# Performance work log

Hardware: AMD Instinct MI355X
Metric: run time of the kernel (lower is better)

## Reference

```python
import jax, jax.numpy as jnp
import numpy as np

HIDDEN = 128

def setup_inputs() -> dict:
    key = jax.random.key(0)
    ks = jax.random.split(key, 12)
    N, T, H = 4096, 64, HIDDEN
    s_in = 1.0 / np.sqrt(2.0)
    s_h = 1.0 / np.sqrt(H)
    return {
        "x_seq": jax.random.normal(ks[0], (N, T), dtype=jnp.float32),
        "m_seq": jax.random.uniform(ks[1], (N, T), dtype=jnp.float32),
        # linear layers stored as [in, out] (math identical to torch x @ W.T + b)
        "W_in": jax.random.normal(ks[2], (2, H), dtype=jnp.float32) * s_in,
        "b_in": jax.random.normal(ks[3], (H,), dtype=jnp.float32) * 0.01,
        "W_proj": jax.random.normal(ks[4], (H, H), dtype=jnp.float32) * s_h,
        "b_proj": jax.random.normal(ks[5], (H,), dtype=jnp.float32) * 0.01,
        "W_gcn": jax.random.normal(ks[6], (H, H), dtype=jnp.float32) * s_h,
        "b_gcn": jax.random.normal(ks[7], (H,), dtype=jnp.float32) * 0.01,
        "W_out": jax.random.normal(ks[8], (H, 1), dtype=jnp.float32) * s_h,
        "b_out": jax.random.normal(ks[9], (1,), dtype=jnp.float32) * 0.01,
    }


def reference(x_seq, m_seq, W_in, b_in, W_proj, b_proj, W_gcn, b_gcn, W_out, b_out):
    N, T = x_seq.shape
    H = W_in.shape[1]
    scale = 1.0 / jnp.sqrt(jnp.asarray(H, dtype=x_seq.dtype))
    # [T, N, 2] time-major inputs for scan
    xs = jnp.stack([x_seq, m_seq], axis=-1).transpose(1, 0, 2)
    h0 = jnp.zeros((N, H), dtype=x_seq.dtype)

    def step(h, inp_t):
        h_in = jax.nn.relu(inp_t @ W_in + b_in)            # [N, H]
        h_proj = h @ W_proj + b_proj                        # [N, H]
        A_dyn = jax.nn.softmax(h_proj @ h_proj.T * scale, axis=1)  # [N, N]
        msg = A_dyn @ h_in                                  # [N, H]
        h_new = jax.nn.relu(msg @ W_gcn + b_gcn + h_in)     # [N, H]
        pred = (h_new @ W_out + b_out)[:, 0]                # [N]
        return h_new, pred

    _, preds = jax.lax.scan(step, h0, xs)  # preds: [T, N]
    return preds.T  # [N, T]
```

## Files before the change

### kernel.cpp

```cpp
#include <hip/hip_runtime.h>
#include <math.h>

#define NN 4096
#define TT 64
#define HH 128
#define NNP 4160
#define SLICE (128 * NNP)
#define SPLITS 8
#define KPB (NN / SPLITS)
#define KT 64
#define NTILES (KPB / KT)
#define QB 64
#define SCALE 0.08838834764831845f
#define CSHIFT 16.0f

typedef __attribute__((ext_vector_type(8))) short short8;
typedef __attribute__((ext_vector_type(4))) float f32x4;
typedef unsigned long long u64;
#define MFMA(a, b, c)   __builtin_amdgcn_mfma_f32_16x16x32_bf16((a), (b), (c), 0, 0, 0)

__device__ __forceinline__ short f2b(float f) {
    union { float f; unsigned u; } v; v.f = f;
    unsigned r = v.u + 0x7fffu + ((v.u >> 16) & 1u);
    return (short)(r >> 16);
}
__device__ __forceinline__ float b2f(short s) {
    union { unsigned u; float f; } v; v.u = ((unsigned)(unsigned short)s) << 16;
    return v.f;
}
__device__ __forceinline__ void lds_fence() {
    __asm__ __volatile__("s_waitcnt lgkmcnt(0)" ::: "memory");
}


__global__ __launch_bounds__(256) void prep_kernel(
    const float* __restrict__ x_seq, const float* __restrict__ m_seq,
    const float* __restrict__ W_in,  const float* __restrict__ b_in,
    const float* __restrict__ W_proj,const float* __restrict__ b_proj,
    const float* __restrict__ W_gcn,
    short* __restrict__ hp, short* __restrict__ hinT_all,
    short* __restrict__ WgT, short* __restrict__ WpT)
{
    __shared__ __align__(16) short hb[128 * 66];
    const int b = blockIdx.x, tid = threadIdx.x;
    if (b < 256) {
        const int n0 = b * 16;
        for (int i = tid; i < 16 * HH; i += 256) {
            const int q = i >> 7, j = i & 127, n = n0 + q;
            hp[n * HH + j] = f2b(b_proj[j]);
        }
    } else if (b < 272) {
        const int wb = b - 256;
        #pragma unroll
        for (int k = 0; k < 4; ++k) {
            const int idx = wb * 1024 + k * 256 + tid;
            const int n = idx >> 7, kk = idx & 127;
            WgT[idx] = f2b(W_gcn[kk * HH + n]);
            WpT[idx] = f2b(W_proj[kk * HH + n]);
        }
    } else {
        const int u = b - 272;
        const int t = u >> 6, n0 = (u & 63) * 64;
        for (int i = tid; i < 64 * HH; i += 256) {
            const int q = i >> 7, j = i & 127, n = n0 + q;
            float hv = x_seq[n * TT + t] * W_in[j] + m_seq[n * TT + t] * W_in[HH + j] + b_in[j];
            hv = hv > 0.f ? hv : 0.f;
            hb[j * 66 + q] = f2b(hv);
        }
        __syncthreads();
        short* dst = hinT_all + (size_t)t * SLICE;
        for (int c = tid; c < 128 * 16; c += 256) {
            const int j = c >> 4, off = (c & 15) * 4;
            const int nb = n0 + off;
            const int tcol = (nb & ~31) | (((nb >> 2) & 3) << 3) | (((nb >> 4) & 1) << 2);
            const unsigned lo = *(const unsigned*)&hb[j * 66 + off];
            const unsigned hi = *(const unsigned*)&hb[j * 66 + off + 2];
            const u64 v = (u64)lo | ((u64)hi << 32);
            *(u64*)&dst[(size_t)j * NNP + tcol] = v;
        }
    }
}

__global__ __launch_bounds__(256, 2) void attn_kernel(
    const short* __restrict__ hp, const short* __restrict__ hinT,
    short* __restrict__ OpartB, float* __restrict__ lpart)
{
    __shared__ __align__(16) char pool[71680];
    short* KtS = (short*)pool;
    short* VtS = (short*)(pool + 34816);

    const int tid  = threadIdx.x;
    const int wave = tid >> 6, lane = tid & 63;
    const int ln = lane & 15, g = lane >> 4;
    const int split = blockIdx.x >> 6, qg = blockIdx.x & 63;
    const int q0 = qg * QB + wave * 16;
    const int kbase = split * KPB;

    const int krow = tid >> 4, kcol = (tid & 15) * 8;
    const int vrow = tid >> 3, vcol = (tid & 7) * 8;

    short8 qf[4];
    #pragma unroll
    for (int kc = 0; kc < 4; ++kc)
        qf[kc] = *(const short8*)&hp[(q0 + ln) * HH + kc * 32 + g * 8];

    f32x4 oacc[8] = {};
    f32x4 lacc = {};
    short8 vone;
    #pragma unroll
    for (int e = 0; e < 8; ++e) vone[e] = (short)0x3F80;

    short8 ksA[4], vsA[4];
    auto load_tile = [&](int kt_) {
        const int kb = kbase + kt_ * KT;
        #pragma unroll
        for (int k = 0; k < 4; ++k)
            ksA[k] = *(const short8*)&hp[(kb + krow + 16 * k) * HH + kcol];
        #pragma unroll
        for (int k = 0; k < 4; ++k)
            vsA[k] = *(const short8*)&hinT[(size_t)(vrow + 32 * k) * NNP + kb + vcol];
    };
    auto store_tile = [&](int b) {
        #pragma unroll
        for (int k = 0; k < 4; ++k)
            *(short8*)&KtS[b * 8704 + (krow + 16 * k) * 136 + kcol] = ksA[k];
        #pragma unroll
        for (int k = 0; k < 4; ++k)
            *(short8*)&VtS[b * 9216 + (vrow + 32 * k) * 72 + vcol] = vsA[k];
    };

    load_tile(0);
    store_tile(0);

    for (int kt = 0; kt < NTILES; ++kt) {
        const int b = kt & 1;
        __syncthreads();

        short8 kf[4][4];
        #pragma unroll
        for (int kt2 = 0; kt2 < 4; ++kt2)
            #pragma unroll
            for (int kc = 0; kc < 4; ++kc)
                kf[kt2][kc] = *(const short8*)&KtS[b * 8704 + (kt2 * 16 + ln) * 136 + kc * 32 + g * 8];

        if (kt + 1 < NTILES) load_tile(kt + 1);

        f32x4 st[4] = {};
        __builtin_amdgcn_s_setprio(1);
        #pragma unroll
        for (int kt2 = 0; kt2 < 4; ++kt2)
            #pragma unroll
            for (int kc = 0; kc < 4; ++kc)
                st[kt2] = MFMA(kf[kt2][kc], qf[kc], st[kt2]);
        __builtin_amdgcn_s_setprio(0);

        short8 pa[2];
        #pragma unroll
        for (int p = 0; p < 2; ++p) {
            short8 paq;
            #pragma unroll
            for (int e = 0; e < 8; ++e) {
                const float s = (e < 4) ? st[2 * p][e] : st[2 * p + 1][e - 4];
                paq[e] = f2b(__expf(s * SCALE - CSHIFT));
            }
            pa[p] = paq;
        }

        if (kt + 1 < NTILES) store_tile(b ^ 1);

        #pragma unroll
        for (int p = 0; p < 2; ++p) {
            short8 vf[8];
            #pragma unroll
            for (int dt = 0; dt < 8; ++dt)
                vf[dt] = *(const short8*)&VtS[b * 9216 + (dt * 16 + ln) * 72 + p * 32 + g * 8];
            __builtin_amdgcn_s_setprio(1);
            #pragma unroll
            for (int dt = 0; dt < 8; ++dt)
                oacc[dt] = MFMA(pa[p], vf[dt], oacc[dt]);
            lacc = MFMA(pa[p], vone, lacc);
            __builtin_amdgcn_s_setprio(0);
        }
    }

    __syncthreads();

    if (ln == 0) {
        #pragma unroll
        for (int r = 0; r < 4; ++r)
            lpart[split * NN + q0 + g * 4 + r] = lacc[r];
    }

    short* bounce = (short*)pool + wave * 2048;
    #pragma unroll
    for (int dt = 0; dt < 8; ++dt)
        #pragma unroll
        for (int r = 0; r < 4; ++r)
            bounce[(g * 4 + r) * 128 + dt * 16 + ln] = f2b(oacc[dt][r]);
    lds_fence();
    #pragma unroll
    for (int sub = 0; sub < 4; ++sub) {
        const int qrow = sub * 4 + (lane >> 4), chunk = lane & 15;
        const short8 rd = *(const short8*)&bounce[qrow * 128 + chunk * 8];
        *(short8*)&OpartB[((size_t)split * NN + q0 + qrow) * HH + chunk * 8] = rd;
    }
}

__global__ __launch_bounds__(512) void fuse_kernel(
    const short* __restrict__ OpartB, const float* __restrict__ lpart,
    short* __restrict__ hp,
    const short* __restrict__ WgT, const short* __restrict__ WpT,
    const float* __restrict__ b_gcn, const float* __restrict__ b_proj,
    const float* __restrict__ W_out, const float* __restrict__ b_out,
    const float* __restrict__ x_seq, const float* __restrict__ m_seq,
    const float* __restrict__ W_in,  const float* __restrict__ b_in,
    float* __restrict__ out, int t)
{
    __shared__ __align__(16) short msgb[16 * 136];
    __shared__ __align__(16) short hnb[16 * 136];
    __shared__ float larr[16];
    __shared__ float ppd[8 * 16];

    const int tid = threadIdx.x;
    const int wave = tid >> 6, lane = tid & 63;
    const int ln = lane & 15, g = lane >> 4;
    const int fb = blockIdx.x;
    const int qg64 = (fb & 7) + 8 * (fb >> 5);
    const int qb = qg64 * 64 + ((fb >> 3) & 3) * 16;

    if (tid < 16) {
        float l = 0.f;
        #pragma unroll
        for (int sp = 0; sp < SPLITS; ++sp) l += lpart[sp * NN + qb + tid];
        larr[tid] = 1.0f / l;
    }
    __syncthreads();

    if (tid < 256) {
        const int q = tid >> 4, c8 = (tid & 15) * 8;
        float s[8] = {0.f, 0.f, 0.f, 0.f, 0.f, 0.f, 0.f, 0.f};
        #pragma unroll
        for (int sp = 0; sp < SPLITS; ++sp) {
            const short8 v = *(const short8*)&OpartB[((size_t)sp * NN + qb + q) * HH + c8];
            #pragma unroll
            for (int k = 0; k < 8; ++k) s[k] += b2f(v[k]);
        }
        const float inv = larr[q];
        short* mp = &msgb[q * 136 + c8];
        #pragma unroll
        for (int k = 0; k < 8; ++k) mp[k] = f2b(s[k] * inv);
    }
    __syncthreads();

    {
        short8 af[4];
        #pragma unroll
        for (int kc = 0; kc < 4; ++kc)
            af[kc] = *(const short8*)&msgb[ln * 136 + kc * 32 + g * 8];
        f32x4 c = {};
        #pragma unroll
        for (int kc = 0; kc < 4; ++kc)
            c = MFMA(af[kc], *(const short8*)&WgT[(wave * 16 + ln) * HH + kc * 32 + g * 8], c);
        const int j = wave * 16 + ln;
        const float bg = b_gcn[j], wo = W_out[j];
        const float wj0 = W_in[j], wj1 = W_in[HH + j], bj = b_in[j];
        float pr[4];
        #pragma unroll
        for (int r = 0; r < 4; ++r) {
            const int q = g * 4 + r;
            float hv = x_seq[(qb + q) * TT + t] * wj0 + m_seq[(qb + q) * TT + t] * wj1 + bj;
            hv = hv > 0.f ? hv : 0.f;
            float v = c[r] + bg + b2f(f2b(hv));
            v = v > 0.f ? v : 0.f;
            hnb[q * 136 + j] = f2b(v);
            pr[r] = v * wo;
        }
        #pragma unroll
        for (int r = 0; r < 4; ++r) {
            float p = pr[r];
            p += __shfl_xor(p, 1); p += __shfl_xor(p, 2);
            p += __shfl_xor(p, 4); p += __shfl_xor(p, 8);
            if (ln == 0) ppd[wave * 16 + g * 4 + r] = p;
        }
    }
    __syncthreads();

    if (tid < 16) {
        float s = b_out[0];
        #pragma unroll
        for (int w = 0; w < 8; ++w) s += ppd[w * 16 + tid];
        out[(qb + tid) * TT + t] = s;
    }

    if (t < TT - 1) {
        short8 hf[4];
        #pragma unroll
        for (int kc = 0; kc < 4; ++kc)
            hf[kc] = *(const short8*)&hnb[ln * 136 + kc * 32 + g * 8];
        f32x4 c = {};
        #pragma unroll
        for (int kc = 0; kc < 4; ++kc)
            c = MFMA(hf[kc], *(const short8*)&WpT[(wave * 16 + ln) * HH + kc * 32 + g * 8], c);
        const float bp = b_proj[wave * 16 + ln];
        #pragma unroll
        for (int r = 0; r < 4; ++r)
            hp[(qb + g * 4 + r) * HH + wave * 16 + ln] = f2b(c[r] + bp);
    }
}

extern "C" void kernel_launch(void* const* d_in, const int* in_sizes, int n_in,
                              void* d_out, int out_size, void* d_ws, size_t ws_size,
                              hipStream_t stream) {
    const float* x_seq  = (const float*)d_in[0];
    const float* m_seq  = (const float*)d_in[1];
    const float* W_in   = (const float*)d_in[2];
    const float* b_in   = (const float*)d_in[3];
    const float* W_proj = (const float*)d_in[4];
    const float* b_proj = (const float*)d_in[5];
    const float* W_gcn  = (const float*)d_in[6];
    const float* b_gcn  = (const float*)d_in[7];
    const float* W_out  = (const float*)d_in[8];
    const float* b_out  = (const float*)d_in[9];
    float* out = (float*)d_out;

    char* base = (char*)d_ws;
    const size_t MB = 1 << 20;
    short* hp       = (short*)(base + 0 * MB);
    short* WgT      = (short*)(base + 3 * MB);
    short* WpT      = (short*)(base + 3 * MB + 32768);
    float* lpart    = (float*)(base + 3 * MB + 65536);
    short* OpartB   = (short*)(base + 4 * MB);
    short* hinT_all = (short*)(base + 32 * MB);

    prep_kernel<<<272 + 64 * 64, 256, 0, stream>>>(x_seq, m_seq, W_in, b_in,
                                                   W_proj, b_proj, W_gcn,
                                                   hp, hinT_all, WgT, WpT);

    for (int t = 0; t < TT; ++t) {
        const short* hinT_t = hinT_all + (size_t)t * SLICE;
        attn_kernel<<<(NN / QB) * SPLITS, 256, 0, stream>>>(hp, hinT_t, OpartB, lpart);
        fuse_kernel<<<NN / 16, 512, 0, stream>>>(OpartB, lpart, hp,
                                                 WgT, WpT, b_gcn, b_proj, W_out, b_out,
                                                 x_seq, m_seq, W_in, b_in, out, t);
    }
}
```

Baseline: 1.545 ms.

## Process two query tiles per wave and double key splits in attention

Each wave now handles 32 query rows (two 16-row tiles) instead of 16, so every K/V fragment read from LDS feeds twice as many MFMAs. The QK and PV phases are interleaved per 32-key half, which keeps the score registers small. The key dimension is split 16 ways instead of 8 to keep the grid size the same. In exchange, register pressure rises from doubled accumulators, and the fuse kernel must reduce twice as many partial outputs.

```diff
diff --git a/kernel.cpp b/kernel.cpp
--- a/kernel.cpp
+++ b/kernel.cpp
@@ -6,11 +6,11 @@
 #define HH 128
 #define NNP 4160
 #define SLICE (128 * NNP)
-#define SPLITS 8
+#define SPLITS 16
 #define KPB (NN / SPLITS)
 #define KT 64
 #define NTILES (KPB / KT)
-#define QB 64
+#define QB 128
 #define SCALE 0.08838834764831845f
 #define CSHIFT 16.0f
 
@@ -92,20 +92,22 @@
     const int tid  = threadIdx.x;
     const int wave = tid >> 6, lane = tid & 63;
     const int ln = lane & 15, g = lane >> 4;
-    const int split = blockIdx.x >> 6, qg = blockIdx.x & 63;
-    const int q0 = qg * QB + wave * 16;
+    const int split = blockIdx.x >> 5, qg = blockIdx.x & 31;
+    const int q0 = qg * QB + wave * 32;
     const int kbase = split * KPB;
 
     const int krow = tid >> 4, kcol = (tid & 15) * 8;
     const int vrow = tid >> 3, vcol = (tid & 7) * 8;
 
-    short8 qf[4];
+    short8 qf[2][4];
     #pragma unroll
-    for (int kc = 0; kc < 4; ++kc)
-        qf[kc] = *(const short8*)&hp[(q0 + ln) * HH + kc * 32 + g * 8];
-
-    f32x4 oacc[8] = {};
-    f32x4 lacc = {};
+    for (int qt = 0; qt < 2; ++qt)
+        #pragma unroll
+        for (int kc = 0; kc < 4; ++kc)
+            qf[qt][kc] = *(const short8*)&hp[(q0 + qt * 16 + ln) * HH + kc * 32 + g * 8];
+
+    f32x4 oacc[2][8] = {};
+    f32x4 lacc[2] = {};
     short8 vone;
     #pragma unroll
     for (int e = 0; e < 8; ++e) vone[e] = (short)0x3F80;
@@ -136,73 +138,84 @@
         const int b = kt & 1;
         __syncthreads();
 
-        short8 kf[4][4];
-        #pragma unroll
-        for (int kt2 = 0; kt2 < 4; ++kt2)
-            #pragma unroll
-            for (int kc = 0; kc < 4; ++kc)
-                kf[kt2][kc] = *(const short8*)&KtS[b * 8704 + (kt2 * 16 + ln) * 136 + kc * 32 + g * 8];
-
         if (kt + 1 < NTILES) load_tile(kt + 1);
 
-        f32x4 st[4] = {};
-        __builtin_amdgcn_s_setprio(1);
-        #pragma unroll
-        for (int kt2 = 0; kt2 < 4; ++kt2)
-            #pragma unroll
-            for (int kc = 0; kc < 4; ++kc)
-                st[kt2] = MFMA(kf[kt2][kc], qf[kc], st[kt2]);
-        __builtin_amdgcn_s_setprio(0);
-
-        short8 pa[2];
         #pragma unroll
         for (int p = 0; p < 2; ++p) {
-            short8 paq;
-            #pragma unroll
-            for (int e = 0; e < 8; ++e) {
-                const float s = (e < 4) ? st[2 * p][e] : st[2 * p + 1][e - 4];
-                paq[e] = f2b(__expf(s * SCALE - CSHIFT));
+            short8 kf[2][4];
+            #pragma unroll
+            for (int kt2 = 0; kt2 < 2; ++kt2)
+                #pragma unroll
+                for (int kc = 0; kc < 4; ++kc)
+                    kf[kt2][kc] = *(const short8*)&KtS[b * 8704 + ((p * 2 + kt2) * 16 + ln) * 136 + kc * 32 + g * 8];
+
+            f32x4 st[2][2] = {};
+            __builtin_amdgcn_s_setprio(1);
+            #pragma unroll
+            for (int kt2 = 0; kt2 < 2; ++kt2)
+                #pragma unroll
+                for (int qt = 0; qt < 2; ++qt)
+                    #pragma unroll
+                    for (int kc = 0; kc < 4; ++kc)
+                        st[kt2][qt] = MFMA(kf[kt2][kc], qf[qt][kc], st[kt2][qt]);
+            __builtin_amdgcn_s_setprio(0);
+
+            short8 pa[2];
+            #pragma unroll
+            for (int qt = 0; qt < 2; ++qt) {
+                short8 paq;
+                #pragma unroll
+                for (int e = 0; e < 8; ++e) {
+                    const float s = (e < 4) ? st[0][qt][e] : st[1][qt][e - 4];
+                    paq[e] = f2b(__expf(s * SCALE - CSHIFT));
+                }
+                pa[qt] = paq;
             }
-            pa[p] = paq;
-        }
-
-        if (kt + 1 < NTILES) store_tile(b ^ 1);
-
-        #pragma unroll
-        for (int p = 0; p < 2; ++p) {
+
+            if (p == 1 && kt + 1 < NTILES) store_tile(b ^ 1);
+
             short8 vf[8];
             #pragma unroll
             for (int dt = 0; dt < 8; ++dt)
                 vf[dt] = *(const short8*)&VtS[b * 9216 + (dt * 16 + ln) * 72 + p * 32 + g * 8];
             __builtin_amdgcn_s_setprio(1);
             #pragma unroll
-            for (int dt = 0; dt < 8; ++dt)
-                oacc[dt] = MFMA(pa[p], vf[dt], oacc[dt]);
-            lacc = MFMA(pa[p], vone, lacc);
+            for (int qt = 0; qt < 2; ++qt) {
+                #pragma unroll
+                for (int dt = 0; dt < 8; ++dt)
+                    oacc[qt][dt] = MFMA(pa[qt], vf[dt], oacc[qt][dt]);
+                lacc[qt] = MFMA(pa[qt], vone, lacc[qt]);
+            }
             __builtin_amdgcn_s_setprio(0);
         }
     }
 
     __syncthreads();
 
-    if (ln == 0) {
-        #pragma unroll
-        for (int r = 0; r < 4; ++r)
-            lpart[split * NN + q0 + g * 4 + r] = lacc[r];
-    }
+    #pragma unroll
+    for (int qt = 0; qt < 2; ++qt)
+        if (ln == 0) {
+            #pragma unroll
+            for (int r = 0; r < 4; ++r)
+                lpart[split * NN + q0 + qt * 16 + g * 4 + r] = lacc[qt][r];
+        }
 
     short* bounce = (short*)pool + wave * 2048;
     #pragma unroll
-    for (int dt = 0; dt < 8; ++dt)
-        #pragma unroll
-        for (int r = 0; r < 4; ++r)
-            bounce[(g * 4 + r) * 128 + dt * 16 + ln] = f2b(oacc[dt][r]);
-    lds_fence();
-    #pragma unroll
-    for (int sub = 0; sub < 4; ++sub) {
-        const int qrow = sub * 4 + (lane >> 4), chunk = lane & 15;
-        const short8 rd = *(const short8*)&bounce[qrow * 128 + chunk * 8];
-        *(short8*)&OpartB[((size_t)split * NN + q0 + qrow) * HH + chunk * 8] = rd;
+    for (int qt = 0; qt < 2; ++qt) {
+        #pragma unroll
+        for (int dt = 0; dt < 8; ++dt)
+            #pragma unroll
+            for (int r = 0; r < 4; ++r)
+                bounce[(g * 4 + r) * 128 + dt * 16 + ln] = f2b(oacc[qt][dt][r]);
+        lds_fence();
+        #pragma unroll
+        for (int sub = 0; sub < 4; ++sub) {
+            const int qrow = sub * 4 + (lane >> 4), chunk = lane & 15;
+            const short8 rd = *(const short8*)&bounce[qrow * 128 + chunk * 8];
+            *(short8*)&OpartB[((size_t)split * NN + q0 + qt * 16 + qrow) * HH + chunk * 8] = rd;
+        }
+        lds_fence();
     }
 }
 
@@ -225,8 +238,8 @@
     const int wave = tid >> 6, lane = tid & 63;
     const int ln = lane & 15, g = lane >> 4;
     const int fb = blockIdx.x;
-    const int qg64 = (fb & 7) + 8 * (fb >> 5);
-    const int qb = qg64 * 64 + ((fb >> 3) & 3) * 16;
+    const int qg32 = (fb & 7) + 8 * ((fb >> 6) & 3);
+    const int qb = qg32 * 128 + ((fb >> 3) & 7) * 16;
 
     if (tid < 16) {
         float l = 0.f;
```

Result: no change. 1.547 ms (+0.1%).
